# Kernel tuning notes

Hardware: AMD Instinct MI355X
Metric: run time of the kernel (lower is better)

The kernel has to match this reference:

```python
import jax, jax.numpy as jnp
import numpy as np
import math

D_MODEL = 1024
NUM_HEADS = 16
D_K = D_MODEL // NUM_HEADS
B, S = 4, 2048


def setup_inputs() -> dict:
    key = jax.random.key(0)
    ks = jax.random.split(key, 12)
    q = jax.random.normal(ks[0], (B, S, D_MODEL), dtype=jnp.float32)
    k = jax.random.normal(ks[1], (B, S, D_MODEL), dtype=jnp.float32)
    v = jax.random.normal(ks[2], (B, S, D_MODEL), dtype=jnp.float32)
    # causal mask: True where attention is disallowed (masked_fill semantics)
    mask = jnp.triu(jnp.ones((S, S), dtype=bool), k=1)
    # xavier_uniform_ for projection weights, torch Linear default for biases
    limit = math.sqrt(6.0 / (D_MODEL + D_MODEL))
    def xavier(kk):
        return jax.random.uniform(kk, (D_MODEL, D_MODEL), jnp.float32, -limit, limit)
    blim = 1.0 / math.sqrt(D_MODEL)
    def bias(kk):
        return jax.random.uniform(kk, (D_MODEL,), jnp.float32, -blim, blim)
    return {
        "q": q, "k": k, "v": v, "mask": mask,
        "wq": xavier(ks[3]), "bq": bias(ks[4]),
        "wk": xavier(ks[5]), "bk": bias(ks[6]),
        "wv": xavier(ks[7]), "bv": bias(ks[8]),
        "wo": xavier(ks[9]), "bo": bias(ks[10]),
    }


def reference(q, k, v, mask, wq, bq, wk, bk, wv, bv, wo, bo):
    b = q.shape[0]
    # torch Linear: y = x @ W.T + b
    def proj(x, w, bb):
        return (jnp.einsum('bsd,ed->bse', x, w) + bb).reshape(b, -1, NUM_HEADS, D_K).transpose(0, 2, 1, 3)
    qh = proj(q, wq, bq)  # [B,H,S,d_k]
    kh = proj(k, wk, bk)
    vh = proj(v, wv, bv)
    scores = jnp.einsum('bhqd,bhkd->bhqk', qh, kh) / math.sqrt(D_K)
    scores = jnp.where(mask, jnp.float32(-1e9), scores)
    probs = jax.nn.softmax(scores, axis=-1)  # dropout p=0 -> identity
    out = jnp.einsum('bhqk,bhkd->bhqd', probs, vh)
    out = out.transpose(0, 2, 1, 3).reshape(b, -1, D_MODEL)
    return jnp.einsum('bsd,ed->bse', out, wo) + bo
```

## Files before the change

### kernel.cpp

```cpp
#include <hip/hip_runtime.h>
#include <hip/hip_bf16.h>
#include <math.h>

#define S_LEN 2048
#define DM    1024
#define NH    16
#define DKH   64
#define NEG_BIG (-1e30f)
#define QSCALE 0.18033688f

typedef __bf16 bf16_t;
typedef bf16_t bf16x8 __attribute__((ext_vector_type(8)));
typedef bf16_t bf16x4 __attribute__((ext_vector_type(4)));
typedef bf16_t bf16x2 __attribute__((ext_vector_type(2)));
typedef float  f32x4  __attribute__((ext_vector_type(4)));

__device__ __forceinline__ void gload16(const void* g, void* l) {
    __builtin_amdgcn_global_load_lds((const __attribute__((address_space(1))) void*)g,
                                     (__attribute__((address_space(3))) void*)l, 16, 0, 0);
}

__device__ __forceinline__ unsigned pack2(float a, float b) {
    bf16x2 v; v[0] = (bf16_t)a; v[1] = (bf16_t)b;
    return __builtin_bit_cast(unsigned, v);
}

__device__ __forceinline__ bf16x8 cvt8v(f32x4 a, f32x4 b) {
    bf16x8 v;
    v[0] = (bf16_t)a[0]; v[1] = (bf16_t)a[1]; v[2] = (bf16_t)a[2]; v[3] = (bf16_t)a[3];
    v[4] = (bf16_t)b[0]; v[5] = (bf16_t)b[1]; v[6] = (bf16_t)b[2]; v[7] = (bf16_t)b[3];
    return v;
}

__global__ __launch_bounds__(256) void cvt4_w(const float* __restrict__ w0, const float* __restrict__ w1,
                                              const float* __restrict__ w2, const float* __restrict__ w3,
                                              bf16_t* __restrict__ o0, bf16_t* __restrict__ o1,
                                              bf16_t* __restrict__ o2, bf16_t* __restrict__ o3) {
    const float* in; bf16_t* out;
    switch (blockIdx.y) {
        case 0: in = w0; out = o0; break;
        case 1: in = w1; out = o1; break;
        case 2: in = w2; out = o2; break;
        default: in = w3; out = o3; break;
    }
    int i = (blockIdx.x * 256 + threadIdx.x) * 4;
    float4 f = *(const float4*)(in + i);
    bf16x4 v;
    v[0] = (bf16_t)f.x; v[1] = (bf16_t)f.y; v[2] = (bf16_t)f.z; v[3] = (bf16_t)f.w;
    *(bf16x4*)(out + i) = v;
}

template<int EPI>
__global__ __launch_bounds__(256) void gemm_proj(const float* __restrict__ Af,
                                                 const bf16_t* __restrict__ B,
                                                 const float* __restrict__ bias,
                                                 bf16_t* __restrict__ Out,
                                                 float oscale) {
    __shared__ float  AsF[2][128 * 32];
    __shared__ bf16_t Bs[2][128 * 32];

    const int d    = blockIdx.x;
    const int orig = (d & 7) * 64 + (d >> 3);
    const int mBase = (orig >> 3) * 128;
    const int nBase = (orig & 7) * 128;

    const int tid  = threadIdx.x;
    const int w    = tid >> 6;
    const int lane = tid & 63;
    const int g    = lane >> 4;
    const int r    = lane & 15;
    const int wm   = w >> 1, wn = w & 1;

    const int srow = lane >> 2;
    const int scol = (lane & 3) * 8;
    const int frow = lane >> 3;
    const int fsl  = (lane & 7) ^ (frow & 7);

    auto stage = [&](int buf, int kt) {
        #pragma unroll
        for (int c = 0; c < 4; ++c) {
            const int row = w * 32 + c * 8;
            gload16(Af + (size_t)(mBase + row + frow) * 1024 + kt + fsl * 4, &AsF[buf][row * 32]);
        }
        #pragma unroll
        for (int c = 0; c < 2; ++c) {
            const int row = w * 32 + c * 16;
            gload16(B + (size_t)(nBase + row + srow) * 1024 + kt + scol, &Bs[buf][row * 32]);
        }
    };

    f32x4 acc[4][4] = {};

    stage(0, 0);
    asm volatile("s_waitcnt vmcnt(0)" ::: "memory");
    __builtin_amdgcn_s_barrier();

    int cur = 0;
    for (int kt = 0; kt < 1024; kt += 32) {
        if (kt + 32 < 1024) stage(cur ^ 1, kt + 32);

        bf16x8 af[4], bfr[4];
        #pragma unroll
        for (int i = 0; i < 4; i++) {
            const int R = wm * 64 + i * 16 + r;
            const float* rb = &AsF[cur][R * 32];
            f32x4 f0 = *(const f32x4*)(rb + (((2 * g) ^ (r & 7)) << 2));
            f32x4 f1 = *(const f32x4*)(rb + (((2 * g + 1) ^ (r & 7)) << 2));
            af[i] = cvt8v(f0, f1);
        }
        #pragma unroll
        for (int i = 0; i < 4; i++)
            bfr[i] = *(const bf16x8*)&Bs[cur][(wn * 64 + i * 16 + r) * 32 + g * 8];

        #pragma unroll
        for (int mi = 0; mi < 4; mi++)
            #pragma unroll
            for (int ni = 0; ni < 4; ni++)
                acc[mi][ni] = __builtin_amdgcn_mfma_f32_16x16x32_bf16(
                    af[mi], bfr[ni], acc[mi][ni], 0, 0, 0);

        asm volatile("s_waitcnt vmcnt(0)" ::: "memory");
        __builtin_amdgcn_s_barrier();
        cur ^= 1;
    }

    #pragma unroll
    for (int ni = 0; ni < 4; ni++) {
        const int n = nBase + wn * 64 + ni * 16 + r;
        const float bn = bias[n];
        #pragma unroll
        for (int mi = 0; mi < 4; mi++) {
            #pragma unroll
            for (int qq = 0; qq < 4; qq++) {
                int m = mBase + wm * 64 + mi * 16 + g * 4 + qq;
                float val = (acc[mi][ni][qq] + bn) * oscale;
                int b = m >> 11, s = m & 2047;
                int hh = n >> 6, dd = n & 63;
                bf16_t bvv = (bf16_t)val;
                if constexpr (EPI == 0)
                    Out[(((size_t)(b * NH + hh)) * S_LEN + s) * DKH + dd] = bvv;
                else
                    Out[(((size_t)(b * NH + hh)) * DKH + dd) * S_LEN + s] = bvv;
            }
        }
    }
}

__global__ __launch_bounds__(256) void gemm_o(const bf16_t* __restrict__ A,
                                              const bf16_t* __restrict__ B,
                                              const float* __restrict__ bias,
                                              float* __restrict__ Out) {
    __shared__ bf16_t As[2][128 * 32];
    __shared__ bf16_t Bs[2][128 * 32];

    const int d    = blockIdx.x;
    const int orig = (d & 7) * 64 + (d >> 3);
    const int mBase = (orig >> 3) * 128;
    const int nBase = (orig & 7) * 128;

    const int tid  = threadIdx.x;
    const int w    = tid >> 6;
    const int lane = tid & 63;
    const int g    = lane >> 4;
    const int r    = lane & 15;
    const int wm   = w >> 1, wn = w & 1;

    const int srow = lane >> 2;
    const int scol = (lane & 3) * 8;

    auto stage = [&](int buf, int kt) {
        #pragma unroll
        for (int c = 0; c < 2; ++c) {
            const int row = w * 32 + c * 16;
            gload16(A + (size_t)(mBase + row + srow) * 1024 + kt + scol, &As[buf][row * 32]);
            gload16(B + (size_t)(nBase + row + srow) * 1024 + kt + scol, &Bs[buf][row * 32]);
        }
    };

    f32x4 acc[4][4] = {};

    stage(0, 0);
    asm volatile("s_waitcnt vmcnt(0)" ::: "memory");
    __builtin_amdgcn_s_barrier();

    int cur = 0;
    for (int kt = 0; kt < 1024; kt += 32) {
        if (kt + 32 < 1024) stage(cur ^ 1, kt + 32);

        bf16x8 af[4], bfr[4];
        #pragma unroll
        for (int i = 0; i < 4; i++)
            af[i] = *(const bf16x8*)&As[cur][(wm * 64 + i * 16 + r) * 32 + g * 8];
        #pragma unroll
        for (int i = 0; i < 4; i++)
            bfr[i] = *(const bf16x8*)&Bs[cur][(wn * 64 + i * 16 + r) * 32 + g * 8];

        #pragma unroll
        for (int mi = 0; mi < 4; mi++)
            #pragma unroll
            for (int ni = 0; ni < 4; ni++)
                acc[mi][ni] = __builtin_amdgcn_mfma_f32_16x16x32_bf16(
                    af[mi], bfr[ni], acc[mi][ni], 0, 0, 0);

        asm volatile("s_waitcnt vmcnt(0)" ::: "memory");
        __builtin_amdgcn_s_barrier();
        cur ^= 1;
    }

    #pragma unroll
    for (int ni = 0; ni < 4; ni++) {
        const int n = nBase + wn * 64 + ni * 16 + r;
        const float bn = bias[n];
        #pragma unroll
        for (int mi = 0; mi < 4; mi++) {
            #pragma unroll
            for (int qq = 0; qq < 4; qq++) {
                int m = mBase + wm * 64 + mi * 16 + g * 4 + qq;
                Out[(size_t)m * 1024 + n] = acc[mi][ni][qq] + bn;
            }
        }
    }
}

__device__ __forceinline__ void tile_softmax(f32x4 s[4], bool diag, int kbase, int qg,
                                             int g, int srcA, int srcB, bool hi,
                                             bf16x8 pf[2]) {
    unsigned P32[8];
    #pragma unroll
    for (int ni = 0; ni < 4; ++ni) {
        float p[4];
        #pragma unroll
        for (int e = 0; e < 4; ++e) {
            float xx = s[ni][e];
            if (diag) {
                int kk = kbase + ni * 16 + g * 4 + e;
                if (kk > qg) xx = NEG_BIG;
            }
            p[e] = __builtin_amdgcn_exp2f(xx);
        }
        P32[2 * ni]     = pack2(p[0], p[1]);
        P32[2 * ni + 1] = pack2(p[2], p[3]);
    }
    unsigned A0 = __shfl(P32[0], srcA), A1 = __shfl(P32[1], srcA);
    unsigned A2 = __shfl(P32[2], srcA), A3 = __shfl(P32[3], srcA);
    unsigned A4 = __shfl(P32[4], srcA), A5 = __shfl(P32[5], srcA);
    unsigned A6 = __shfl(P32[6], srcA), A7 = __shfl(P32[7], srcA);
    unsigned B0 = __shfl(P32[0], srcB), B1 = __shfl(P32[1], srcB);
    unsigned B2 = __shfl(P32[2], srcB), B3 = __shfl(P32[3], srcB);
    unsigned B4 = __shfl(P32[4], srcB), B5 = __shfl(P32[5], srcB);
    unsigned B6 = __shfl(P32[6], srcB), B7 = __shfl(P32[7], srcB);
    union U { unsigned u[4]; bf16x8 v; } u0, u1;
    u0.u[0] = hi ? A2 : A0;  u0.u[1] = hi ? A3 : A1;
    u0.u[2] = hi ? B2 : B0;  u0.u[3] = hi ? B3 : B1;
    u1.u[0] = hi ? A6 : A4;  u1.u[1] = hi ? A7 : A5;
    u1.u[2] = hi ? B6 : B4;  u1.u[3] = hi ? B7 : B5;
    pf[0] = u0.v;
    pf[1] = u1.v;
}

__global__ __launch_bounds__(256) void attn8_kernel(const bf16_t* __restrict__ Qh,
                                                    const bf16_t* __restrict__ Kh,
                                                    const bf16_t* __restrict__ Vt,
                                                    bf16_t* __restrict__ Out) {
    __shared__ bf16_t KV[2][2][64][64];

    const int j   = blockIdx.x;
    const int c   = j >> 8;
    const int rem = j & 255;
    const int y   = rem >> 6;
    const int bh  = rem & 63;
    const int p   = (c == 0) ? y : (c == 1) ? 15 - y : (c == 2) ? 4 + y : 11 - y;

    const int b   = bh >> 4, h = bh & 15;
    const int tid = threadIdx.x;
    const int w    = tid >> 6;
    const int lane = tid & 63;
    const int g    = lane >> 4;
    const int r    = lane & 15;

    const int qtA = 2 * p, qtB = 2 * p + 1, last = qtB;

    const int srcA = 32 * (g & 1) + r;
    const int srcB = srcA + 16;
    const bool hi  = (g >= 2);

    const bf16_t* Qg = Qh + (size_t)bh * S_LEN * DKH;
    const bf16_t* Kg = Kh + (size_t)bh * S_LEN * DKH;
    const bf16_t* Vg = Vt + (size_t)bh * DKH * S_LEN;

    const int qA = qtA * 64 + w * 16 + r;
    const int qB = qtB * 64 + w * 16 + r;

    bf16x8 qfA[2], qfB[2];
    #pragma unroll
    for (int hh = 0; hh < 2; ++hh) {
        qfA[hh] = *(const bf16x8*)(Qg + (size_t)qA * DKH + hh * 32 + g * 8);
        qfB[hh] = *(const bf16x8*)(Qg + (size_t)qB * DKH + hh * 32 + g * 8);
    }

    bf16x8 ones;
    #pragma unroll
    for (int jj = 0; jj < 8; ++jj) ones[jj] = (bf16_t)1.0f;

    auto stage = [&](int buf, int kt) {
        #pragma unroll
        for (int cc = 0; cc < 2; ++cc) {
            const int row = w * 16 + cc * 8 + (lane >> 3);
            const int sl  = (lane & 7) ^ (row & 7);
            gload16(Kg + ((size_t)(kt * 64 + row)) * DKH + sl * 8,
                    (char*)&KV[buf][0][0][0] + w * 2048 + cc * 1024);
            gload16(Vg + (size_t)row * S_LEN + kt * 64 + sl * 8,
                    (char*)&KV[buf][1][0][0] + w * 2048 + cc * 1024);
        }
    };

    f32x4 oA[4] = {}, oB[4] = {};
    f32x4 lA4 = {}, lB4 = {};

    stage(0, 0);
    asm volatile("s_waitcnt vmcnt(0)" ::: "memory");
    __builtin_amdgcn_s_barrier();

    for (int kt = 0; kt <= last; ++kt) {
        const int buf = kt & 1;
        if (kt < last) stage(buf ^ 1, kt + 1);

        bf16x8 kf[4][2];
        #pragma unroll
        for (int ni = 0; ni < 4; ++ni) {
            const int row = ni * 16 + r;
            const char* base = (const char*)&KV[buf][0][0][0] + (row << 7);
            kf[ni][0] = *(const bf16x8*)(base + (((0 + g) ^ (row & 7)) << 4));
            kf[ni][1] = *(const bf16x8*)(base + (((4 + g) ^ (row & 7)) << 4));
        }

        const bool actA = (kt <= qtA);
        bf16x8 pfA[2], pfB[2];

        if (actA) {
            f32x4 s[4] = {};
            __builtin_amdgcn_s_setprio(1);
            #pragma unroll
            for (int ni = 0; ni < 4; ++ni) {
                s[ni] = __builtin_amdgcn_mfma_f32_16x16x32_bf16(kf[ni][0], qfA[0], s[ni], 0, 0, 0);
                s[ni] = __builtin_amdgcn_mfma_f32_16x16x32_bf16(kf[ni][1], qfA[1], s[ni], 0, 0, 0);
            }
            __builtin_amdgcn_s_setprio(0);
            tile_softmax(s, kt == qtA, kt * 64, qA, g, srcA, srcB, hi, pfA);
        }
        {
            f32x4 s[4] = {};
            __builtin_amdgcn_s_setprio(1);
            #pragma unroll
            for (int ni = 0; ni < 4; ++ni) {
                s[ni] = __builtin_amdgcn_mfma_f32_16x16x32_bf16(kf[ni][0], qfB[0], s[ni], 0, 0, 0);
                s[ni] = __builtin_amdgcn_mfma_f32_16x16x32_bf16(kf[ni][1], qfB[1], s[ni], 0, 0, 0);
            }
            __builtin_amdgcn_s_setprio(0);
            tile_softmax(s, kt == qtB, kt * 64, qB, g, srcA, srcB, hi, pfB);
        }

        __builtin_amdgcn_s_setprio(1);
        #pragma unroll
        for (int ndi = 0; ndi < 4; ++ndi) {
            const int row = ndi * 16 + r;
            const char* base = (const char*)&KV[buf][1][0][0] + (row << 7);
            bf16x8 v0 = *(const bf16x8*)(base + (((0 + g) ^ (row & 7)) << 4));
            bf16x8 v1 = *(const bf16x8*)(base + (((4 + g) ^ (row & 7)) << 4));
            if (actA) {
                oA[ndi] = __builtin_amdgcn_mfma_f32_16x16x32_bf16(v0, pfA[0], oA[ndi], 0, 0, 0);
                oA[ndi] = __builtin_amdgcn_mfma_f32_16x16x32_bf16(v1, pfA[1], oA[ndi], 0, 0, 0);
            }
            oB[ndi] = __builtin_amdgcn_mfma_f32_16x16x32_bf16(v0, pfB[0], oB[ndi], 0, 0, 0);
            oB[ndi] = __builtin_amdgcn_mfma_f32_16x16x32_bf16(v1, pfB[1], oB[ndi], 0, 0, 0);
        }
        if (actA) {
            lA4 = __builtin_amdgcn_mfma_f32_16x16x32_bf16(ones, pfA[0], lA4, 0, 0, 0);
            lA4 = __builtin_amdgcn_mfma_f32_16x16x32_bf16(ones, pfA[1], lA4, 0, 0, 0);
        }
        lB4 = __builtin_amdgcn_mfma_f32_16x16x32_bf16(ones, pfB[0], lB4, 0, 0, 0);
        lB4 = __builtin_amdgcn_mfma_f32_16x16x32_bf16(ones, pfB[1], lB4, 0, 0, 0);
        __builtin_amdgcn_s_setprio(0);

        asm volatile("s_waitcnt vmcnt(0)" ::: "memory");
        __builtin_amdgcn_s_barrier();
    }

    const float invA = 1.0f / lA4[0], invB = 1.0f / lB4[0];
    bf16_t* OutA = Out + ((size_t)(b * S_LEN + qA)) * DM + h * DKH;
    bf16_t* OutB = Out + ((size_t)(b * S_LEN + qB)) * DM + h * DKH;
    #pragma unroll
    for (int ndi = 0; ndi < 4; ++ndi) {
        bf16x4 pa, pb;
        #pragma unroll
        for (int e = 0; e < 4; ++e) {
            pa[e] = (bf16_t)(oA[ndi][e] * invA);
            pb[e] = (bf16_t)(oB[ndi][e] * invB);
        }
        *(bf16x4*)(OutA + ndi * 16 + g * 4) = pa;
        *(bf16x4*)(OutB + ndi * 16 + g * 4) = pb;
    }
}

extern "C" void kernel_launch(void* const* d_in, const int* in_sizes, int n_in,
                              void* d_out, int out_size, void* d_ws, size_t ws_size,
                              hipStream_t stream) {
    const float* q  = (const float*)d_in[0];
    const float* k  = (const float*)d_in[1];
    const float* v  = (const float*)d_in[2];
    const float* wq = (const float*)d_in[4];
    const float* bq = (const float*)d_in[5];
    const float* wk = (const float*)d_in[6];
    const float* bk = (const float*)d_in[7];
    const float* wv = (const float*)d_in[8];
    const float* bv = (const float*)d_in[9];
    const float* wo = (const float*)d_in[10];
    const float* bo = (const float*)d_in[11];
    float* out = (float*)d_out;

    bf16_t* ws   = (bf16_t*)d_ws;
    bf16_t* Wq   = ws;
    bf16_t* Wk   = Wq + (1 << 20);
    bf16_t* Wv   = Wk + (1 << 20);
    bf16_t* Wo   = Wv + (1 << 20);
    bf16_t* Qh   = Wo + (1 << 20);
    bf16_t* Kh   = Qh + (8 << 20);
    bf16_t* Vt   = Kh + (8 << 20);
    bf16_t* attn = Vt + (8 << 20);

    cvt4_w<<<dim3(1024, 4), 256, 0, stream>>>(wq, wk, wv, wo, Wq, Wk, Wv, Wo);

    gemm_proj<0><<<512, 256, 0, stream>>>(q, Wq, bq, Qh, QSCALE);
    gemm_proj<0><<<512, 256, 0, stream>>>(k, Wk, bk, Kh, 1.0f);
    gemm_proj<1><<<512, 256, 0, stream>>>(v, Wv, bv, Vt, 1.0f);

    attn8_kernel<<<1024, 256, 0, stream>>>(Qh, Kh, Vt, attn);

    gemm_o<<<512, 256, 0, stream>>>(attn, Wo, bo, out);
}
```

Measured before the change: 192.3 us.

## Triple-buffer LDS staging in projection and output GEMMs with prefetch depth two

Both GEMM kernels move from double to triple LDS buffers and now issue global-to-LDS loads two K-tiles ahead. A partial vmcnt wait replaces the full drain, so the next tile's loads stay in flight during compute. Each iteration now needs one barrier instead of two phases. In exchange, LDS use per block grows (about 72KB for the projection GEMM), which may reduce how many blocks fit per CU.

```diff
diff --git a/kernel.cpp b/kernel.cpp
--- a/kernel.cpp
+++ b/kernel.cpp
@@ -56,8 +56,8 @@
                                                  const float* __restrict__ bias,
                                                  bf16_t* __restrict__ Out,
                                                  float oscale) {
-    __shared__ float  AsF[2][128 * 32];
-    __shared__ bf16_t Bs[2][128 * 32];
+    __shared__ float  AsF[3][128 * 32];
+    __shared__ bf16_t Bs[3][128 * 32];
 
     const int d    = blockIdx.x;
     const int orig = (d & 7) * 64 + (d >> 3);
@@ -89,40 +89,43 @@
         }
     };
 
-    f32x4 acc[4][4] = {};
-
-    stage(0, 0);
-    asm volatile("s_waitcnt vmcnt(0)" ::: "memory");
-    __builtin_amdgcn_s_barrier();
-
-    int cur = 0;
-    for (int kt = 0; kt < 1024; kt += 32) {
-        if (kt + 32 < 1024) stage(cur ^ 1, kt + 32);
-
+    auto compute = [&](int buf, f32x4 (*acc)[4]) {
         bf16x8 af[4], bfr[4];
         #pragma unroll
         for (int i = 0; i < 4; i++) {
             const int R = wm * 64 + i * 16 + r;
-            const float* rb = &AsF[cur][R * 32];
+            const float* rb = &AsF[buf][R * 32];
             f32x4 f0 = *(const f32x4*)(rb + (((2 * g) ^ (r & 7)) << 2));
             f32x4 f1 = *(const f32x4*)(rb + (((2 * g + 1) ^ (r & 7)) << 2));
             af[i] = cvt8v(f0, f1);
         }
         #pragma unroll
         for (int i = 0; i < 4; i++)
-            bfr[i] = *(const bf16x8*)&Bs[cur][(wn * 64 + i * 16 + r) * 32 + g * 8];
-
+            bfr[i] = *(const bf16x8*)&Bs[buf][(wn * 64 + i * 16 + r) * 32 + g * 8];
         #pragma unroll
         for (int mi = 0; mi < 4; mi++)
             #pragma unroll
             for (int ni = 0; ni < 4; ni++)
                 acc[mi][ni] = __builtin_amdgcn_mfma_f32_16x16x32_bf16(
                     af[mi], bfr[ni], acc[mi][ni], 0, 0, 0);
-
-        asm volatile("s_waitcnt vmcnt(0)" ::: "memory");
+    };
+
+    f32x4 acc[4][4] = {};
+
+    stage(0, 0);
+    stage(1, 32);
+
+    int cur = 0;
+    for (int t = 0; t < 31; ++t) {
+        asm volatile("s_waitcnt vmcnt(6)" ::: "memory");
         __builtin_amdgcn_s_barrier();
-        cur ^= 1;
-    }
+        compute(cur, acc);
+        if (t + 2 < 32) stage((cur + 2) % 3, (t + 2) * 32);
+        cur = (cur + 1) % 3;
+    }
+    asm volatile("s_waitcnt vmcnt(0)" ::: "memory");
+    __builtin_amdgcn_s_barrier();
+    compute(cur, acc);
 
     #pragma unroll
     for (int ni = 0; ni < 4; ni++) {
@@ -150,8 +153,8 @@
                                               const bf16_t* __restrict__ B,
                                               const float* __restrict__ bias,
                                               float* __restrict__ Out) {
-    __shared__ bf16_t As[2][128 * 32];
-    __shared__ bf16_t Bs[2][128 * 32];
+    __shared__ bf16_t As[3][128 * 32];
+    __shared__ bf16_t Bs[3][128 * 32];
 
     const int d    = blockIdx.x;
     const int orig = (d & 7) * 64 + (d >> 3);
@@ -177,35 +180,38 @@
         }
     };
 
-    f32x4 acc[4][4] = {};
-
-    stage(0, 0);
-    asm volatile("s_waitcnt vmcnt(0)" ::: "memory");
-    __builtin_amdgcn_s_barrier();
-
-    int cur = 0;
-    for (int kt = 0; kt < 1024; kt += 32) {
-        if (kt + 32 < 1024) stage(cur ^ 1, kt + 32);
-
+    auto compute = [&](int buf, f32x4 (*acc)[4]) {
         bf16x8 af[4], bfr[4];
         #pragma unroll
         for (int i = 0; i < 4; i++)
-            af[i] = *(const bf16x8*)&As[cur][(wm * 64 + i * 16 + r) * 32 + g * 8];
+            af[i] = *(const bf16x8*)&As[buf][(wm * 64 + i * 16 + r) * 32 + g * 8];
         #pragma unroll
         for (int i = 0; i < 4; i++)
-            bfr[i] = *(const bf16x8*)&Bs[cur][(wn * 64 + i * 16 + r) * 32 + g * 8];
-
+            bfr[i] = *(const bf16x8*)&Bs[buf][(wn * 64 + i * 16 + r) * 32 + g * 8];
         #pragma unroll
         for (int mi = 0; mi < 4; mi++)
             #pragma unroll
             for (int ni = 0; ni < 4; ni++)
                 acc[mi][ni] = __builtin_amdgcn_mfma_f32_16x16x32_bf16(
                     af[mi], bfr[ni], acc[mi][ni], 0, 0, 0);
-
-        asm volatile("s_waitcnt vmcnt(0)" ::: "memory");
+    };
+
+    f32x4 acc[4][4] = {};
+
+    stage(0, 0);
+    stage(1, 32);
+
+    int cur = 0;
+    for (int t = 0; t < 31; ++t) {
+        asm volatile("s_waitcnt vmcnt(4)" ::: "memory");
         __builtin_amdgcn_s_barrier();
-        cur ^= 1;
-    }
+        compute(cur, acc);
+        if (t + 2 < 32) stage((cur + 2) % 3, (t + 2) * 32);
+        cur = (cur + 1) % 3;
+    }
+    asm volatile("s_waitcnt vmcnt(0)" ::: "memory");
+    __builtin_amdgcn_s_barrier();
+    compute(cur, acc);
 
     #pragma unroll
     for (int ni = 0; ni < 4; ni++) {
```

After: 182.3 us. -5.2%, faster.
